# Performance work log

Hardware: AMD Instinct MI355X
Metric: run time of the kernel (lower is better)

The kernel has to match this reference:

```python
import jax, jax.numpy as jnp
import numpy as np

B, C, H, W = 8192, 2048, 2, 2
CR = C // 16
EPS = 1e-5

def setup_inputs() -> dict:
    key = jax.random.key(0)
    ks = jax.random.split(key, 8)
    x = jax.random.normal(ks[0], (B, C, H, W), dtype=jnp.float32)
    gamma = jax.random.normal(ks[1], (C,), dtype=jnp.float32) * 0.1 + 1.0
    beta = jax.random.normal(ks[2], (C,), dtype=jnp.float32) * 0.1
    mean = jax.random.normal(ks[3], (C,), dtype=jnp.float32) * 0.1
    var = jax.random.uniform(ks[4], (C,), dtype=jnp.float32, minval=0.5, maxval=1.5)
    w1 = jax.random.normal(ks[5], (CR, C), dtype=jnp.float32) * (1.0 / np.sqrt(C))
    b1 = jnp.zeros((CR,), dtype=jnp.float32)
    w2 = jax.random.normal(ks[6], (C, CR), dtype=jnp.float32) * (1.0 / np.sqrt(CR))
    b2 = jnp.zeros((C,), dtype=jnp.float32)
    return {"x": x, "gamma": gamma, "beta": beta, "mean": mean, "var": var,
            "w1": w1, "b1": b1, "w2": w2, "b2": b2}

def reference(x, gamma, beta, mean, var, w1, b1, w2, b2):
    # BatchNorm (inference form) + ReLU, over [B,C,H,W]
    inv = gamma * jax.lax.rsqrt(var + EPS)           # [C]
    xn = jax.nn.relu(x * inv[None, :, None, None]
                     + (beta - mean * inv)[None, :, None, None])
    # global average pool -> [B, C]
    p = jnp.mean(xn, axis=(2, 3))
    # two 1x1 convs on [B,C,1,1] == channel MLP
    h = jax.nn.relu(jnp.einsum('bc,rc->br', p, w1) + b1)   # [B, C/16]
    g = jax.nn.sigmoid(jnp.einsum('br,cr->bc', h, w2) + b2) # [B, C]
    # repeat(1,1,2,2) then in-place add == broadcast add over 2x2 spatial
    return x + g[:, :, None, None]
```

## Files before the change

kernel.cpp:

```cpp
#include <hip/hip_runtime.h>


typedef unsigned short u16;
typedef unsigned int u32;
typedef short short8 __attribute__((ext_vector_type(8)));
typedef __bf16 bf16x8 __attribute__((ext_vector_type(8)));
typedef unsigned short ushort4v __attribute__((ext_vector_type(4)));
typedef float floatx4 __attribute__((ext_vector_type(4)));
typedef float floatx2 __attribute__((ext_vector_type(2)));

#define C_CH 2048
#define NB 8
#define THREADS 512
#define PROW 2056
#define HROW 136

__device__ __forceinline__ float bf2f(u16 u) {
    u32 v = ((u32)u) << 16;
    return __builtin_bit_cast(float, v);
}
__device__ __forceinline__ u16 f2bf(float f) {
    u32 v = __builtin_bit_cast(u32, f);
    v = (v + 0x7FFFu + ((v >> 16) & 1u)) >> 16;
    return (u16)v;
}
__device__ __forceinline__ bf16x8 ld8(const u16* p) {
    short8 s = *(const short8*)p;
    return __builtin_bit_cast(bf16x8, s);
}
__device__ __forceinline__ bf16x8 cvt8(floatx4 a, floatx4 b) {
    short8 s;
    s[0] = (short)f2bf(a[0]); s[1] = (short)f2bf(a[1]);
    s[2] = (short)f2bf(a[2]); s[3] = (short)f2bf(a[3]);
    s[4] = (short)f2bf(b[0]); s[5] = (short)f2bf(b[1]);
    s[6] = (short)f2bf(b[2]); s[7] = (short)f2bf(b[3]);
    return __builtin_bit_cast(bf16x8, s);
}
__device__ __forceinline__ bool is_bf16_data(const u16* var_raw) {
    int ok = 1;
    #pragma unroll
    for (int i = 0; i < 8; ++i) {
        u16 u = var_raw[2 * i];
        ok &= (u >= 0x3F00u) && (u <= 0x3FC0u);
    }
    return ok != 0;
}

extern "C" __global__ void __launch_bounds__(THREADS, 8)
se_fused(const void* __restrict__ x_raw,
         const void* __restrict__ gamma_raw,
         const void* __restrict__ beta_raw,
         const void* __restrict__ mean_raw,
         const void* __restrict__ var_raw,
         const void* __restrict__ w1_raw,
         const void* __restrict__ b1_raw,
         const void* __restrict__ w2_raw,
         const void* __restrict__ b2_raw,
         void* __restrict__ out_raw) {
    __shared__ u16 p_lds[NB * PROW];
    __shared__ u16 h_lds[NB * HROW];

    const int tid  = threadIdx.x;
    const int lane = tid & 63;
    const int wv   = tid >> 6;
    const int quad = lane >> 4;
    const int l16  = lane & 15;
    const long b0  = (long)blockIdx.x * NB;

    const bool bf = is_bf16_data((const u16*)var_raw);

    {
        const int cA = tid << 1;
        const int cB = cA + 1024;
        float gmA0, gmA1, btA0, btA1, mnA0, mnA1, vrA0, vrA1;
        float gmB0, gmB1, btB0, btB1, mnB0, mnB1, vrB0, vrB1;
        if (bf) {
            const u16 *gu = (const u16*)gamma_raw, *bu = (const u16*)beta_raw,
                      *mu = (const u16*)mean_raw,  *vu = (const u16*)var_raw;
            u32 t;
            t = *(const u32*)(gu + cA); gmA0 = bf2f((u16)t); gmA1 = bf2f((u16)(t >> 16));
            t = *(const u32*)(bu + cA); btA0 = bf2f((u16)t); btA1 = bf2f((u16)(t >> 16));
            t = *(const u32*)(mu + cA); mnA0 = bf2f((u16)t); mnA1 = bf2f((u16)(t >> 16));
            t = *(const u32*)(vu + cA); vrA0 = bf2f((u16)t); vrA1 = bf2f((u16)(t >> 16));
            t = *(const u32*)(gu + cB); gmB0 = bf2f((u16)t); gmB1 = bf2f((u16)(t >> 16));
            t = *(const u32*)(bu + cB); btB0 = bf2f((u16)t); btB1 = bf2f((u16)(t >> 16));
            t = *(const u32*)(mu + cB); mnB0 = bf2f((u16)t); mnB1 = bf2f((u16)(t >> 16));
            t = *(const u32*)(vu + cB); vrB0 = bf2f((u16)t); vrB1 = bf2f((u16)(t >> 16));
        } else {
            const float *gf = (const float*)gamma_raw, *bfp = (const float*)beta_raw,
                        *mf = (const float*)mean_raw,  *vf = (const float*)var_raw;
            floatx2 t2;
            t2 = *(const floatx2*)(gf  + cA); gmA0 = t2[0]; gmA1 = t2[1];
            t2 = *(const floatx2*)(bfp + cA); btA0 = t2[0]; btA1 = t2[1];
            t2 = *(const floatx2*)(mf  + cA); mnA0 = t2[0]; mnA1 = t2[1];
            t2 = *(const floatx2*)(vf  + cA); vrA0 = t2[0]; vrA1 = t2[1];
            t2 = *(const floatx2*)(gf  + cB); gmB0 = t2[0]; gmB1 = t2[1];
            t2 = *(const floatx2*)(bfp + cB); btB0 = t2[0]; btB1 = t2[1];
            t2 = *(const floatx2*)(mf  + cB); mnB0 = t2[0]; mnB1 = t2[1];
            t2 = *(const floatx2*)(vf  + cB); vrB0 = t2[0]; vrB1 = t2[1];
        }
        const float invA0 = gmA0 * rsqrtf(vrA0 + 1e-5f), bsA0 = btA0 - mnA0 * invA0;
        const float invA1 = gmA1 * rsqrtf(vrA1 + 1e-5f), bsA1 = btA1 - mnA1 * invA1;
        const float invB0 = gmB0 * rsqrtf(vrB0 + 1e-5f), bsB0 = btB0 - mnB0 * invB0;
        const float invB1 = gmB1 * rsqrtf(vrB1 + 1e-5f), bsB1 = btB1 - mnB1 * invB1;

        if (bf) {
            const short8* x8b = (const short8*)((const u16*)x_raw + b0 * 8192);
            #pragma unroll 2
            for (int m = 0; m < NB; ++m) {
                short8 xa = x8b[(m << 10) + tid];
                short8 xb = x8b[(m << 10) + 512 + tid];
                float sA0 = 0.f, sA1 = 0.f, sB0 = 0.f, sB1 = 0.f;
                #pragma unroll
                for (int j = 0; j < 4; ++j) {
                    sA0 += fmaxf(fmaf(bf2f((u16)xa[j]),     invA0, bsA0), 0.f);
                    sA1 += fmaxf(fmaf(bf2f((u16)xa[4 + j]), invA1, bsA1), 0.f);
                    sB0 += fmaxf(fmaf(bf2f((u16)xb[j]),     invB0, bsB0), 0.f);
                    sB1 += fmaxf(fmaf(bf2f((u16)xb[4 + j]), invB1, bsB1), 0.f);
                }
                *(u32*)(&p_lds[m * PROW + cA]) =
                    (u32)f2bf(sA0 * 0.25f) | ((u32)f2bf(sA1 * 0.25f) << 16);
                *(u32*)(&p_lds[m * PROW + cB]) =
                    (u32)f2bf(sB0 * 0.25f) | ((u32)f2bf(sB1 * 0.25f) << 16);
            }
        } else {
            const floatx4* x4f = (const floatx4*)x_raw + b0 * 2048;
            #pragma unroll 2
            for (int m = 0; m < NB; ++m) {
                int ia = (m << 10) + tid;
                int ib = ia + 512;
                floatx4 a0 = x4f[2 * ia], a1 = x4f[2 * ia + 1];
                floatx4 c0 = x4f[2 * ib], c1 = x4f[2 * ib + 1];
                float sA0 = 0.f, sA1 = 0.f, sB0 = 0.f, sB1 = 0.f;
                #pragma unroll
                for (int j = 0; j < 4; ++j) {
                    sA0 += fmaxf(fmaf(a0[j], invA0, bsA0), 0.f);
                    sA1 += fmaxf(fmaf(a1[j], invA1, bsA1), 0.f);
                    sB0 += fmaxf(fmaf(c0[j], invB0, bsB0), 0.f);
                    sB1 += fmaxf(fmaf(c1[j], invB1, bsB1), 0.f);
                }
                *(u32*)(&p_lds[m * PROW + cA]) =
                    (u32)f2bf(sA0 * 0.25f) | ((u32)f2bf(sA1 * 0.25f) << 16);
                *(u32*)(&p_lds[m * PROW + cB]) =
                    (u32)f2bf(sB0 * 0.25f) | ((u32)f2bf(sB1 * 0.25f) << 16);
            }
        }
    }
    __syncthreads();

    const int rr = (wv << 4) | l16;
    {
        floatx4 acc = {0.f, 0.f, 0.f, 0.f};
        const u16* pp = p_lds + (l16 & 7) * PROW + (quad << 3);
        if (bf) {
            const u16* w1p = (const u16*)w1_raw + (long)rr * C_CH + (quad << 3);
            #pragma unroll 4
            for (int k0 = 0; k0 < C_CH; k0 += 32)
                acc = __builtin_amdgcn_mfma_f32_16x16x32_bf16(ld8(pp + k0), ld8(w1p + k0), acc, 0, 0, 0);
        } else {
            const float* w1p = (const float*)w1_raw + (long)rr * C_CH + (quad << 3);
            #pragma unroll 2
            for (int k0 = 0; k0 < C_CH; k0 += 32) {
                floatx4 wa = *(const floatx4*)(w1p + k0);
                floatx4 wb = *(const floatx4*)(w1p + k0 + 4);
                acc = __builtin_amdgcn_mfma_f32_16x16x32_bf16(ld8(pp + k0), cvt8(wa, wb), acc, 0, 0, 0);
            }
        }
        float bb = bf ? bf2f(((const u16*)b1_raw)[rr]) : ((const float*)b1_raw)[rr];
        if (quad < 2) {
            #pragma unroll
            for (int r = 0; r < 4; ++r) {
                int m = (quad << 2) | r;
                h_lds[m * HROW + rr] = f2bf(fmaxf(acc[r] + bb, 0.f));
            }
        }
    }
    __syncthreads();

    bf16x8 af[4];
    #pragma unroll
    for (int kk = 0; kk < 4; ++kk)
        af[kk] = ld8(h_lds + (l16 & 7) * HROW + (kk << 5) + (quad << 3));

    const ushort4v* x4u = (const ushort4v*)x_raw;
    ushort4v*       o4u = (ushort4v*)out_raw;
    const floatx4*  x4f = (const floatx4*)x_raw;
    floatx4*        o4f = (floatx4*)out_raw;

    for (int i = 0; i < 16; ++i) {
        int c = (wv * 16 + i) * 16 + l16;
        floatx4 a2 = {0.f, 0.f, 0.f, 0.f};
        if (bf) {
            const u16* w2p = (const u16*)w2_raw + (long)c * 128 + (quad << 3);
            #pragma unroll
            for (int kk = 0; kk < 4; ++kk)
                a2 = __builtin_amdgcn_mfma_f32_16x16x32_bf16(af[kk], ld8(w2p + (kk << 5)), a2, 0, 0, 0);
        } else {
            const float* w2p = (const float*)w2_raw + (long)c * 128 + (quad << 3);
            #pragma unroll
            for (int kk = 0; kk < 4; ++kk) {
                floatx4 wa = *(const floatx4*)(w2p + (kk << 5));
                floatx4 wb = *(const floatx4*)(w2p + (kk << 5) + 4);
                a2 = __builtin_amdgcn_mfma_f32_16x16x32_bf16(af[kk], cvt8(wa, wb), a2, 0, 0, 0);
            }
        }
        float zb = bf ? bf2f(((const u16*)b2_raw)[c]) : ((const float*)b2_raw)[c];
        if (quad < 2) {
            #pragma unroll
            for (int r = 0; r < 4; ++r) {
                int m = (quad << 2) | r;
                float z = a2[r] + zb;
                float g = 1.f / (1.f + __expf(-z));
                long idx = (b0 + m) * 2048 + c;
                if (bf) {
                    ushort4v xv = x4u[idx];
                    ushort4v ov;
                    #pragma unroll
                    for (int j = 0; j < 4; ++j) ov[j] = f2bf(bf2f(xv[j]) + g);
                    o4u[idx] = ov;
                } else {
                    floatx4 xv = x4f[idx];
                    floatx4 ov;
                    #pragma unroll
                    for (int j = 0; j < 4; ++j) ov[j] = xv[j] + g;
                    o4f[idx] = ov;
                }
            }
        }
    }
}

extern "C" void kernel_launch(void* const* d_in, const int* in_sizes, int n_in,
                              void* d_out, int out_size, void* d_ws, size_t ws_size,
                              hipStream_t stream) {
    se_fused<<<dim3(8192 / NB), dim3(THREADS), 0, stream>>>(
        d_in[0], d_in[1], d_in[2], d_in[3], d_in[4],
        d_in[5], d_in[6], d_in[7], d_in[8], d_out);
}
```

Baseline: 674.3 us.

## Pre-convert SE MLP weights to bf16 in workspace with separate prep kernel

Adds a small prep kernel that converts w1/w2 to bf16 and the biases to fp32 in the workspace buffer. The main kernel then reads these prepared weights directly as MFMA operands, so each of the 1024 blocks no longer converts fp32 weights itself. It also uses nontemporal loads and stores for the final broadcast-add pass and simplifies the BN-stat loading. It adds a second launch and only runs when the workspace is large enough; otherwise it falls back to the old kernel.

```diff
diff --git a/kernel.cpp b/kernel.cpp
--- a/kernel.cpp
+++ b/kernel.cpp
@@ -15,6 +15,10 @@
 #define PROW 2056
 #define HROW 136
 
+#define WS_W2_OFF   (128 * 2048)
+#define WS_B1_BYTE  (1u << 20)
+#define WS_NEED     ((size_t)(1u << 20) + 512 + 2048 * 4)
+
 __device__ __forceinline__ float bf2f(u16 u) {
     u32 v = ((u32)u) << 16;
     return __builtin_bit_cast(float, v);
@@ -46,17 +50,209 @@
     return ok != 0;
 }
 
+extern "C" __global__ void __launch_bounds__(256)
+se_convw(const void* __restrict__ w1_raw, const void* __restrict__ b1_raw,
+         const void* __restrict__ w2_raw, const void* __restrict__ b2_raw,
+         const void* __restrict__ var_raw, void* __restrict__ ws) {
+    const bool bf = is_bf16_data((const u16*)var_raw);
+    u16* w1b = (u16*)ws;
+    u16* w2b = w1b + WS_W2_OFF;
+    float* b1f = (float*)((char*)ws + WS_B1_BYTE);
+    float* b2f = b1f + 128;
+    int gid = blockIdx.x * 256 + threadIdx.x;
+    if (bf) {
+        const ushort4v* s1 = (const ushort4v*)w1_raw;
+        const ushort4v* s2 = (const ushort4v*)w2_raw;
+        *(ushort4v*)(w1b + gid * 4) = s1[gid];
+        *(ushort4v*)(w2b + gid * 4) = s2[gid];
+        if (gid < 128)  b1f[gid] = bf2f(((const u16*)b1_raw)[gid]);
+        if (gid < 2048) b2f[gid] = bf2f(((const u16*)b2_raw)[gid]);
+    } else {
+        const floatx4* s1 = (const floatx4*)w1_raw;
+        const floatx4* s2 = (const floatx4*)w2_raw;
+        floatx4 a = s1[gid], b = s2[gid];
+        ushort4v o1, o2;
+        #pragma unroll
+        for (int j = 0; j < 4; ++j) { o1[j] = f2bf(a[j]); o2[j] = f2bf(b[j]); }
+        *(ushort4v*)(w1b + gid * 4) = o1;
+        *(ushort4v*)(w2b + gid * 4) = o2;
+        if (gid < 128)  b1f[gid] = ((const float*)b1_raw)[gid];
+        if (gid < 2048) b2f[gid] = ((const float*)b2_raw)[gid];
+    }
+}
+
 extern "C" __global__ void __launch_bounds__(THREADS, 8)
-se_fused(const void* __restrict__ x_raw,
-         const void* __restrict__ gamma_raw,
-         const void* __restrict__ beta_raw,
-         const void* __restrict__ mean_raw,
-         const void* __restrict__ var_raw,
-         const void* __restrict__ w1_raw,
-         const void* __restrict__ b1_raw,
-         const void* __restrict__ w2_raw,
-         const void* __restrict__ b2_raw,
-         void* __restrict__ out_raw) {
+se_main(const void* __restrict__ x_raw,
+        const void* __restrict__ gamma_raw,
+        const void* __restrict__ beta_raw,
+        const void* __restrict__ mean_raw,
+        const void* __restrict__ var_raw,
+        const void* __restrict__ ws,
+        void* __restrict__ out_raw) {
+    __shared__ u16 p_lds[NB * PROW];
+    __shared__ u16 h_lds[NB * HROW];
+
+    const int tid  = threadIdx.x;
+    const int lane = tid & 63;
+    const int wv   = tid >> 6;
+    const int quad = lane >> 4;
+    const int l16  = lane & 15;
+    const long b0  = (long)blockIdx.x * NB;
+
+    const u16*   w1b = (const u16*)ws;
+    const u16*   w2b = w1b + WS_W2_OFF;
+    const float* b1f = (const float*)((const char*)ws + WS_B1_BYTE);
+    const float* b2f = b1f + 128;
+
+    const bool bf = is_bf16_data((const u16*)var_raw);
+
+    {
+        float inv[4], bs[4];
+        if (bf) {
+            const u16 *gu = (const u16*)gamma_raw, *bu = (const u16*)beta_raw,
+                      *mu = (const u16*)mean_raw,  *vu = (const u16*)var_raw;
+            #pragma unroll
+            for (int k = 0; k < 4; ++k) {
+                int c = tid + 512 * k;
+                float g = bf2f(gu[c]), bb = bf2f(bu[c]);
+                float mm = bf2f(mu[c]), vv = bf2f(vu[c]);
+                inv[k] = g * rsqrtf(vv + 1e-5f);
+                bs[k]  = bb - mm * inv[k];
+            }
+        } else {
+            const float *gf = (const float*)gamma_raw, *bfp = (const float*)beta_raw,
+                        *mf = (const float*)mean_raw,  *vf = (const float*)var_raw;
+            #pragma unroll
+            for (int k = 0; k < 4; ++k) {
+                int c = tid + 512 * k;
+                inv[k] = gf[c] * rsqrtf(vf[c] + 1e-5f);
+                bs[k]  = bfp[c] - mf[c] * inv[k];
+            }
+        }
+        if (bf) {
+            const ushort4v* xr = (const ushort4v*)x_raw + b0 * 2048;
+            #pragma unroll 2
+            for (int m = 0; m < NB; ++m) {
+                #pragma unroll
+                for (int k = 0; k < 4; ++k) {
+                    int c = tid + 512 * k;
+                    ushort4v u = xr[m * 2048 + c];
+                    float s = 0.f;
+                    #pragma unroll
+                    for (int j = 0; j < 4; ++j)
+                        s += fmaxf(fmaf(bf2f(u[j]), inv[k], bs[k]), 0.f);
+                    p_lds[m * PROW + c] = f2bf(s * 0.25f);
+                }
+            }
+        } else {
+            const floatx4* xr = (const floatx4*)x_raw + b0 * 2048;
+            #pragma unroll 2
+            for (int m = 0; m < NB; ++m) {
+                #pragma unroll
+                for (int k = 0; k < 4; ++k) {
+                    int c = tid + 512 * k;
+                    floatx4 v = xr[m * 2048 + c];
+                    float s = 0.f;
+                    #pragma unroll
+                    for (int j = 0; j < 4; ++j)
+                        s += fmaxf(fmaf(v[j], inv[k], bs[k]), 0.f);
+                    p_lds[m * PROW + c] = f2bf(s * 0.25f);
+                }
+            }
+        }
+    }
+    __syncthreads();
+
+    const int rr = (wv << 4) | l16;
+    {
+        floatx4 acc = {0.f, 0.f, 0.f, 0.f};
+        const u16* pp  = p_lds + (l16 & 7) * PROW + (quad << 3);
+        const u16* w1p = w1b + (long)rr * C_CH + (quad << 3);
+        #pragma unroll 4
+        for (int k0 = 0; k0 < C_CH; k0 += 32)
+            acc = __builtin_amdgcn_mfma_f32_16x16x32_bf16(ld8(pp + k0), ld8(w1p + k0), acc, 0, 0, 0);
+        float bb = b1f[rr];
+        if (quad < 2) {
+            #pragma unroll
+            for (int r = 0; r < 4; ++r) {
+                int m = (quad << 2) | r;
+                h_lds[m * HROW + rr] = f2bf(fmaxf(acc[r] + bb, 0.f));
+            }
+        }
+    }
+    __syncthreads();
+
+    {
+        bf16x8 af[4];
+        #pragma unroll
+        for (int kk = 0; kk < 4; ++kk)
+            af[kk] = ld8(h_lds + (l16 & 7) * HROW + (kk << 5) + (quad << 3));
+
+        #pragma unroll 2
+        for (int i = 0; i < 16; ++i) {
+            int c = (wv * 16 + i) * 16 + l16;
+            floatx4 a2 = {0.f, 0.f, 0.f, 0.f};
+            const u16* w2p = w2b + (long)c * 128 + (quad << 3);
+            #pragma unroll
+            for (int kk = 0; kk < 4; ++kk)
+                a2 = __builtin_amdgcn_mfma_f32_16x16x32_bf16(af[kk], ld8(w2p + (kk << 5)), a2, 0, 0, 0);
+            float zb = b2f[c];
+            if (quad < 2) {
+                #pragma unroll
+                for (int r = 0; r < 4; ++r) {
+                    int m = (quad << 2) | r;
+                    float z = a2[r] + zb;
+                    float g = 1.f / (1.f + __expf(-z));
+                    p_lds[m * PROW + c] = f2bf(g);
+                }
+            }
+        }
+    }
+    __syncthreads();
+
+    if (bf) {
+        const short8* xr8 = (const short8*)x_raw + b0 * 1024;
+        short8*       or8 = (short8*)out_raw + b0 * 1024;
+        #pragma unroll 4
+        for (int it = 0; it < 16; ++it) {
+            int j  = (it << 9) | tid;
+            int m  = j >> 10, cc = j & 1023;
+            u32 gg = *(const u32*)(&p_lds[m * PROW + (cc << 1)]);
+            float g0 = bf2f((u16)gg), g1 = bf2f((u16)(gg >> 16));
+            short8 xv = __builtin_nontemporal_load(&xr8[j]);
+            short8 ov;
+            #pragma unroll
+            for (int jj = 0; jj < 4; ++jj) ov[jj] = (short)f2bf(bf2f((u16)xv[jj]) + g0);
+            #pragma unroll
+            for (int jj = 4; jj < 8; ++jj) ov[jj] = (short)f2bf(bf2f((u16)xv[jj]) + g1);
+            __builtin_nontemporal_store(ov, &or8[j]);
+        }
+    } else {
+        const floatx4* xr = (const floatx4*)x_raw + b0 * 2048;
+        floatx4*       orr = (floatx4*)out_raw + b0 * 2048;
+        #pragma unroll 4
+        for (int it = 0; it < 32; ++it) {
+            int j = (it << 9) | tid;
+            int m = j >> 11, c = j & 2047;
+            float g = bf2f(p_lds[m * PROW + c]);
+            floatx4 xv = __builtin_nontemporal_load(&xr[j]);
+            floatx4 ov = {xv[0] + g, xv[1] + g, xv[2] + g, xv[3] + g};
+            __builtin_nontemporal_store(ov, &orr[j]);
+        }
+    }
+}
+
+extern "C" __global__ void __launch_bounds__(THREADS, 8)
+se_legacy(const void* __restrict__ x_raw,
+          const void* __restrict__ gamma_raw,
+          const void* __restrict__ beta_raw,
+          const void* __restrict__ mean_raw,
+          const void* __restrict__ var_raw,
+          const void* __restrict__ w1_raw,
+          const void* __restrict__ b1_raw,
+          const void* __restrict__ w2_raw,
+          const void* __restrict__ b2_raw,
+          void* __restrict__ out_raw) {
     __shared__ u16 p_lds[NB * PROW];
     __shared__ u16 h_lds[NB * HROW];
 
@@ -233,7 +429,14 @@
 extern "C" void kernel_launch(void* const* d_in, const int* in_sizes, int n_in,
                               void* d_out, int out_size, void* d_ws, size_t ws_size,
                               hipStream_t stream) {
-    se_fused<<<dim3(8192 / NB), dim3(THREADS), 0, stream>>>(
-        d_in[0], d_in[1], d_in[2], d_in[3], d_in[4],
-        d_in[5], d_in[6], d_in[7], d_in[8], d_out);
-}
+    if (d_ws != nullptr && ws_size >= WS_NEED) {
+        se_convw<<<dim3(256), dim3(256), 0, stream>>>(
+            d_in[5], d_in[6], d_in[7], d_in[8], d_in[4], d_ws);
+        se_main<<<dim3(8192 / NB), dim3(THREADS), 0, stream>>>(
+            d_in[0], d_in[1], d_in[2], d_in[3], d_in[4], d_ws, d_out);
+    } else {
+        se_legacy<<<dim3(8192 / NB), dim3(THREADS), 0, stream>>>(
+            d_in[0], d_in[1], d_in[2], d_in[3], d_in[4],
+            d_in[5], d_in[6], d_in[7], d_in[8], d_out);
+    }
+}
```

Measured after the change: 544.3 us. 1.24x faster.
